# Performance work log

Measured on AMD Instinct MI355X. Metric: run time of the kernel, lower is better.

## Reference

```python
import jax, jax.numpy as jnp
import numpy as np

POP_LUT = jnp.asarray(np.array([bin(i).count('1') for i in range(256)], dtype=np.float32))


def setup_inputs() -> dict:
    key = jax.random.key(0)
    k1, k2, k3, k4 = jax.random.split(key, 4)
    B, k, H, W, d_v = 4, 8, 64, 64, 32
    z = jax.random.uniform(k1, (B, k, H, W), dtype=jnp.float32)
    evidence_mask = jax.random.randint(k2, (B, H * W), 0, 2).astype(bool)
    value_embed = jax.random.normal(k3, (256, d_v), dtype=jnp.float32)
    mask_value = jax.random.normal(k4, (d_v,), dtype=jnp.float32) * 0.1
    temperature = jnp.asarray(1.0, dtype=jnp.float32)
    return {"z": z, "evidence_mask": evidence_mask, "value_embed": value_embed,
            "mask_value": mask_value, "temperature": temperature}


def _bitpack(z):
    # z: (B, k, H, W) -> codes: (B, N) int32 in [0, 2^k)
    B, k, H, W = z.shape
    bits = (z > 0.5).astype(jnp.int32)
    shifts = (2 ** jnp.arange(k, dtype=jnp.int32)).reshape(1, k, 1, 1)
    return (bits * shifts).sum(axis=1).reshape(B, H * W)


def reference(z, evidence_mask, value_embed, mask_value, temperature):
    B, k, H, W = z.shape
    N = H * W
    d_v = value_embed.shape[1]
    codes = _bitpack(z)                                  # (B, N)
    xor = codes[:, :, None] ^ codes[:, None, :]          # (B, N, N)
    dist = POP_LUT[xor]                                  # Hamming distance via LUT
    temp = jnp.maximum(temperature, 0.1)
    scores = -dist / temp
    # gate: keys without evidence are excluded
    scores = jnp.where(evidence_mask[:, None, :], scores, -jnp.inf)
    # if a batch has zero evidence, fall back to uniform attention (scores=0)
    all_masked = ~jnp.any(evidence_mask, axis=-1)        # (B,)
    scores = jnp.where(all_masked[:, None, None], 0.0, scores)
    attn = jax.nn.softmax(scores, axis=-1)               # (B, N, N)
    values = value_embed[jnp.clip(codes, 0, 255)]        # (B, N, d_v)
    values = jnp.where(evidence_mask[:, :, None], values, mask_value[None, None, :])
    ctx = jnp.einsum('bnm,bmd->bnd', attn, values)       # (B, N, d_v)
    return ctx.transpose(0, 2, 1).reshape(B, d_v, H, W)
```

## Files before the change

kernel.cpp:

```cpp
#include <hip/hip_runtime.h>

#define B_   4
#define K_   8
#define N_   4096
#define DV_  32
#define NC_  256

#define WS_OFF_CODES 65536
#define WS_NEEDED    81920

__device__ __forceinline__ int read_mask(const void* m, int layout, int idx) {
    if (layout == 0) return ((const int*)m)[idx] != 0;
    if (layout == 1) return ((const float*)m)[idx] != 0.0f;
    if (layout == 3) return ((const int*)m)[2 * idx] != 0;
    return ((const unsigned char*)m)[idx] != 0;
}

__device__ __forceinline__ int detect_layout(const void* mask, int tid) {
    __shared__ int ok[3];
    if (tid < 3) ok[tid] = 1;
    __syncthreads();
    const unsigned int* mi = (const unsigned int*)mask;
    int li32 = 1, lf32 = 1, li64 = 1;
    for (int i = tid; i < 4096; i += 256) {
        unsigned int v = mi[i];
        li32 &= (v <= 1u);
        lf32 &= (v == 0u || v == 0x3F800000u);
        li64 &= ((i & 1) ? (v == 0u) : (v <= 1u));
    }
    if (!li32) atomicAnd(&ok[0], 0);
    if (!lf32) atomicAnd(&ok[1], 0);
    if (!li64) atomicAnd(&ok[2], 0);
    __syncthreads();
    return ok[2] ? 3 : (ok[0] ? 0 : (ok[1] ? 1 : 2));
}

__global__ void k1_codes_hist(const float* __restrict__ z, const void* mask,
                              int* __restrict__ part, unsigned char* __restrict__ codes) {
    __shared__ int hist[NC_];
    int tid = threadIdx.x;
    int b = blockIdx.x >> 4;
    int n = ((blockIdx.x & 15) << 8) + tid;
    int layout = detect_layout(mask, tid);
    hist[tid] = 0;
    __syncthreads();
    const float* zb = z + (size_t)b * K_ * N_ + n;
    int code = 0;
#pragma unroll
    for (int j = 0; j < K_; ++j) code |= (zb[j * N_] > 0.5f ? 1 : 0) << j;
    codes[b * N_ + n] = (unsigned char)code;
    if (read_mask(mask, layout, b * N_ + n)) atomicAdd(&hist[code], 1);
    __syncthreads();
    part[blockIdx.x * NC_ + tid] = hist[tid];
}

__global__ void __launch_bounds__(256)
k2_ctx_gather(const int* __restrict__ part, const unsigned char* __restrict__ codes,
              const float* __restrict__ V, const float* __restrict__ mv,
              const float* __restrict__ temperature, float* __restrict__ out) {
    __shared__ float X[NC_ * 33];
    __shared__ float CS[NC_];
    __shared__ int red[4];
    int tid = threadIdx.x;
    int b = blockIdx.x >> 4;
    int n0 = (blockIdx.x & 15) << 8;

    int c = 0;
#pragma unroll
    for (int j = 0; j < 16; ++j) c += part[(b * 16 + j) * NC_ + tid];
    CS[tid] = (float)c;

    int s = c;
#pragma unroll
    for (int off = 32; off; off >>= 1) s += __shfl_down(s, off);
    if ((tid & 63) == 0) red[tid >> 6] = s;
    __syncthreads();
    int evid = red[0] + red[1] + red[2] + red[3];

    float temp = fmaxf(temperature[0], 0.1f);
    float t = __expf(-1.0f / temp);

    for (int i = tid; i < NC_ * 33; i += 256) {
        int cc = i / 33, col = i - cc * 33;
        float cf = CS[cc];
        X[i] = (col < DV_) ? cf * V[cc * DV_ + col] : cf;
    }
    __syncthreads();

#pragma unroll
    for (int stg = 0; stg < 8; ++stg) {
        int bit = 1 << stg;
        for (int p = tid; p < 128 * 33; p += 256) {
            int pi = p / 33, col = p - pi * 33;
            int c0 = ((pi >> stg) << (stg + 1)) | (pi & (bit - 1));
            int i0 = c0 * 33 + col, i1 = i0 + bit * 33;
            float x0 = X[i0], x1 = X[i1];
            X[i0] = fmaf(t, x1, x0);
            X[i1] = fmaf(t, x0, x1);
        }
        __syncthreads();
    }

    int code = codes[b * N_ + n0 + tid];
    float* ob = out + (size_t)b * DV_ * N_ + n0 + tid;
    if (evid == 0) {
#pragma unroll
        for (int d = 0; d < DV_; ++d) ob[d * N_] = mv[d];
    } else {
        float rden = 1.0f / X[code * 33 + DV_];
#pragma unroll
        for (int d = 0; d < DV_; ++d) ob[d * N_] = X[code * 33 + d] * rden;
    }
}

__global__ void __launch_bounds__(1024)
fused_all(const float* __restrict__ z, const void* mask, const float* __restrict__ V,
          const float* __restrict__ mask_value, const float* __restrict__ temperature,
          float* __restrict__ out) {
    __shared__ unsigned short codesL[N_];
    __shared__ float csf[NC_];
    __shared__ int cs[NC_];
    __shared__ float ctxL[NC_ * 33];
    __shared__ int ok[3];
    __shared__ int evid_sh;
    int tid = threadIdx.x;
    int b = blockIdx.x;
    if (tid < 3) ok[tid] = 1;
    if (tid == 0) evid_sh = 0;
    if (tid < NC_) cs[tid] = 0;
    __syncthreads();
    {
        const unsigned int* mi = (const unsigned int*)mask;
        int li32 = 1, lf32 = 1, li64 = 1;
        for (int i = tid; i < 4096; i += 1024) {
            unsigned int v = mi[i];
            li32 &= (v <= 1u);
            lf32 &= (v == 0u || v == 0x3F800000u);
            li64 &= ((i & 1) ? (v == 0u) : (v <= 1u));
        }
        if (!li32) atomicAnd(&ok[0], 0);
        if (!lf32) atomicAnd(&ok[1], 0);
        if (!li64) atomicAnd(&ok[2], 0);
    }
    __syncthreads();
    int layout = ok[2] ? 3 : (ok[0] ? 0 : (ok[1] ? 1 : 2));
    for (int i = tid; i < N_; i += 1024) {
        const float* zb = z + (size_t)b * K_ * N_ + i;
        int code = 0;
#pragma unroll
        for (int j = 0; j < K_; ++j) code |= (zb[j * N_] > 0.5f ? 1 : 0) << j;
        codesL[i] = (unsigned short)code;
        if (read_mask(mask, layout, b * N_ + i)) {
            atomicAdd(&cs[code], 1);
            atomicAdd(&evid_sh, 1);
        }
    }
    __syncthreads();
    if (tid < NC_) csf[tid] = (float)cs[tid];
    __syncthreads();
    int evid = evid_sh;
    float temp = fmaxf(temperature[0], 0.1f);
    float rinv = -1.0f / temp;
    int d = tid & 31;
    for (int qi = 0; qi < 8; ++qi) {
        int q = (qi << 5) + (tid >> 5);
        float num = 0.0f, den = 0.0f;
        for (int c = 0; c < NC_; ++c) {
            float cc = csf[c];
            float w = cc * __expf((float)__popc(q ^ c) * rinv);
            den += w;
            num = fmaf(w, V[c * DV_ + d], num);
        }
        ctxL[q * 33 + d] = (evid == 0) ? mask_value[d] : num / den;
    }
    __syncthreads();
    for (int idx = tid; idx < DV_ * N_; idx += 1024) {
        int dd = idx >> 12;
        int n = idx & (N_ - 1);
        out[(size_t)b * DV_ * N_ + idx] = ctxL[codesL[n] * 33 + dd];
    }
}

extern "C" void kernel_launch(void* const* d_in, const int* in_sizes, int n_in,
                              void* d_out, int out_size, void* d_ws, size_t ws_size,
                              hipStream_t stream) {
    const float* z    = (const float*)d_in[0];
    const void*  mask = d_in[1];
    const float* V    = (const float*)d_in[2];
    const float* mv   = (const float*)d_in[3];
    const float* temp = (const float*)d_in[4];
    float* out = (float*)d_out;

    if (ws_size >= (size_t)WS_NEEDED) {
        char* ws = (char*)d_ws;
        int*           part  = (int*)ws;
        unsigned char* codes = (unsigned char*)(ws + WS_OFF_CODES);
        k1_codes_hist<<<B_ * 16, 256, 0, stream>>>(z, mask, part, codes);
        k2_ctx_gather<<<B_ * 16, 256, 0, stream>>>(part, codes, V, mv, temp, out);
    } else {
        fused_all<<<B_, 1024, 0, stream>>>(z, mask, V, mv, temp, out);
    }
}
```

Before: 29.84 us.

## Fuse histogram and context kernels into one launch with redundant per-block histograms

Replaces the two-kernel pipeline (per-slice partial histograms in a workspace, then a gather kernel) with one kernel. Each of the 64 blocks recomputes the full per-batch code histogram from z and the mask, then runs the butterfly transform and writes its slice. This removes one kernel launch and the workspace round trip, but every block now reads all of its batch's z (16x redundant reads) and builds a 4096-element histogram with shared atomics.

```diff
diff --git a/kernel.cpp b/kernel.cpp
--- a/kernel.cpp
+++ b/kernel.cpp
@@ -5,9 +5,6 @@
 #define N_   4096
 #define DV_  32
 #define NC_  256
-
-#define WS_OFF_CODES 65536
-#define WS_NEEDED    81920
 
 __device__ __forceinline__ int read_mask(const void* m, int layout, int idx) {
     if (layout == 0) return ((const int*)m)[idx] != 0;
@@ -35,41 +32,34 @@
     return ok[2] ? 3 : (ok[0] ? 0 : (ok[1] ? 1 : 2));
 }
 
-__global__ void k1_codes_hist(const float* __restrict__ z, const void* mask,
-                              int* __restrict__ part, unsigned char* __restrict__ codes) {
+__global__ void __launch_bounds__(256)
+fused_one(const float* __restrict__ z, const void* mask, const float* __restrict__ V,
+          const float* __restrict__ mv, const float* __restrict__ temperature,
+          float* __restrict__ out) {
+    __shared__ float X[NC_ * 33];
     __shared__ int hist[NC_];
+    __shared__ int red[4];
     int tid = threadIdx.x;
     int b = blockIdx.x >> 4;
-    int n = ((blockIdx.x & 15) << 8) + tid;
+    int slice = blockIdx.x & 15;
+
     int layout = detect_layout(mask, tid);
     hist[tid] = 0;
     __syncthreads();
-    const float* zb = z + (size_t)b * K_ * N_ + n;
-    int code = 0;
+
+    const float* zb = z + (size_t)b * K_ * N_;
+    int mycode = 0;
+    for (int ci = 0; ci < 16; ++ci) {
+        int n = (ci << 8) + tid;
+        int code = 0;
 #pragma unroll
-    for (int j = 0; j < K_; ++j) code |= (zb[j * N_] > 0.5f ? 1 : 0) << j;
-    codes[b * N_ + n] = (unsigned char)code;
-    if (read_mask(mask, layout, b * N_ + n)) atomicAdd(&hist[code], 1);
+        for (int j = 0; j < K_; ++j) code |= (zb[j * N_ + n] > 0.5f ? 1 : 0) << j;
+        if (ci == slice) mycode = code;
+        if (read_mask(mask, layout, b * N_ + n)) atomicAdd(&hist[code], 1);
+    }
     __syncthreads();
-    part[blockIdx.x * NC_ + tid] = hist[tid];
-}
 
-__global__ void __launch_bounds__(256)
-k2_ctx_gather(const int* __restrict__ part, const unsigned char* __restrict__ codes,
-              const float* __restrict__ V, const float* __restrict__ mv,
-              const float* __restrict__ temperature, float* __restrict__ out) {
-    __shared__ float X[NC_ * 33];
-    __shared__ float CS[NC_];
-    __shared__ int red[4];
-    int tid = threadIdx.x;
-    int b = blockIdx.x >> 4;
-    int n0 = (blockIdx.x & 15) << 8;
-
-    int c = 0;
-#pragma unroll
-    for (int j = 0; j < 16; ++j) c += part[(b * 16 + j) * NC_ + tid];
-    CS[tid] = (float)c;
-
+    int c = hist[tid];
     int s = c;
 #pragma unroll
     for (int off = 32; off; off >>= 1) s += __shfl_down(s, off);
@@ -82,7 +72,7 @@
 
     for (int i = tid; i < NC_ * 33; i += 256) {
         int cc = i / 33, col = i - cc * 33;
-        float cf = CS[cc];
+        float cf = (float)hist[cc];
         X[i] = (col < DV_) ? cf * V[cc * DV_ + col] : cf;
     }
     __syncthreads();
@@ -101,83 +91,14 @@
         __syncthreads();
     }
 
-    int code = codes[b * N_ + n0 + tid];
-    float* ob = out + (size_t)b * DV_ * N_ + n0 + tid;
+    float* ob = out + (size_t)b * DV_ * N_ + (slice << 8) + tid;
     if (evid == 0) {
 #pragma unroll
         for (int d = 0; d < DV_; ++d) ob[d * N_] = mv[d];
     } else {
-        float rden = 1.0f / X[code * 33 + DV_];
+        float rden = 1.0f / X[mycode * 33 + DV_];
 #pragma unroll
-        for (int d = 0; d < DV_; ++d) ob[d * N_] = X[code * 33 + d] * rden;
-    }
-}
-
-__global__ void __launch_bounds__(1024)
-fused_all(const float* __restrict__ z, const void* mask, const float* __restrict__ V,
-          const float* __restrict__ mask_value, const float* __restrict__ temperature,
-          float* __restrict__ out) {
-    __shared__ unsigned short codesL[N_];
-    __shared__ float csf[NC_];
-    __shared__ int cs[NC_];
-    __shared__ float ctxL[NC_ * 33];
-    __shared__ int ok[3];
-    __shared__ int evid_sh;
-    int tid = threadIdx.x;
-    int b = blockIdx.x;
-    if (tid < 3) ok[tid] = 1;
-    if (tid == 0) evid_sh = 0;
-    if (tid < NC_) cs[tid] = 0;
-    __syncthreads();
-    {
-        const unsigned int* mi = (const unsigned int*)mask;
-        int li32 = 1, lf32 = 1, li64 = 1;
-        for (int i = tid; i < 4096; i += 1024) {
-            unsigned int v = mi[i];
-            li32 &= (v <= 1u);
-            lf32 &= (v == 0u || v == 0x3F800000u);
-            li64 &= ((i & 1) ? (v == 0u) : (v <= 1u));
-        }
-        if (!li32) atomicAnd(&ok[0], 0);
-        if (!lf32) atomicAnd(&ok[1], 0);
-        if (!li64) atomicAnd(&ok[2], 0);
-    }
-    __syncthreads();
-    int layout = ok[2] ? 3 : (ok[0] ? 0 : (ok[1] ? 1 : 2));
-    for (int i = tid; i < N_; i += 1024) {
-        const float* zb = z + (size_t)b * K_ * N_ + i;
-        int code = 0;
-#pragma unroll
-        for (int j = 0; j < K_; ++j) code |= (zb[j * N_] > 0.5f ? 1 : 0) << j;
-        codesL[i] = (unsigned short)code;
-        if (read_mask(mask, layout, b * N_ + i)) {
-            atomicAdd(&cs[code], 1);
-            atomicAdd(&evid_sh, 1);
-        }
-    }
-    __syncthreads();
-    if (tid < NC_) csf[tid] = (float)cs[tid];
-    __syncthreads();
-    int evid = evid_sh;
-    float temp = fmaxf(temperature[0], 0.1f);
-    float rinv = -1.0f / temp;
-    int d = tid & 31;
-    for (int qi = 0; qi < 8; ++qi) {
-        int q = (qi << 5) + (tid >> 5);
-        float num = 0.0f, den = 0.0f;
-        for (int c = 0; c < NC_; ++c) {
-            float cc = csf[c];
-            float w = cc * __expf((float)__popc(q ^ c) * rinv);
-            den += w;
-            num = fmaf(w, V[c * DV_ + d], num);
-        }
-        ctxL[q * 33 + d] = (evid == 0) ? mask_value[d] : num / den;
-    }
-    __syncthreads();
-    for (int idx = tid; idx < DV_ * N_; idx += 1024) {
-        int dd = idx >> 12;
-        int n = idx & (N_ - 1);
-        out[(size_t)b * DV_ * N_ + idx] = ctxL[codesL[n] * 33 + dd];
+        for (int d = 0; d < DV_; ++d) ob[d * N_] = X[mycode * 33 + d] * rden;
     }
 }
 
@@ -190,14 +111,5 @@
     const float* mv   = (const float*)d_in[3];
     const float* temp = (const float*)d_in[4];
     float* out = (float*)d_out;
-
-    if (ws_size >= (size_t)WS_NEEDED) {
-        char* ws = (char*)d_ws;
-        int*           part  = (int*)ws;
-        unsigned char* codes = (unsigned char*)(ws + WS_OFF_CODES);
-        k1_codes_hist<<<B_ * 16, 256, 0, stream>>>(z, mask, part, codes);
-        k2_ctx_gather<<<B_ * 16, 256, 0, stream>>>(part, codes, V, mv, temp, out);
-    } else {
-        fused_all<<<B_, 1024, 0, stream>>>(z, mask, V, mv, temp, out);
-    }
+    fused_one<<<B_ * 16, 256, 0, stream>>>(z, mask, V, mv, temp, out);
 }
```

Result: slower. 33.35 us (+11.7%).

## Fuse histogram and context kernels into one cooperative launch with grid sync

Applied to the files above, without the earlier changes.

Merges the two-kernel pipeline (per-slice histograms, then Walsh-transform context and gather) into a single cooperative kernel that uses a grid-wide barrier between phases. Each thread keeps its own code in a register, so the codes no longer round-trip through workspace, and one launch gap is removed. It also rewrites the X initialization so each thread fills its own row directly from registers instead of through the shared count array. In exchange it depends on cooperative-launch support and pays for a grid sync; if the launch fails it falls back to the two-kernel path.

```diff
diff --git a/kernel.cpp b/kernel.cpp
--- a/kernel.cpp
+++ b/kernel.cpp
@@ -1,4 +1,7 @@
 #include <hip/hip_runtime.h>
+#include <hip/hip_cooperative_groups.h>
+
+namespace cg = cooperative_groups;
 
 #define B_   4
 #define K_   8
@@ -7,7 +10,8 @@
 #define NC_  256
 
 #define WS_OFF_CODES 65536
-#define WS_NEEDED    81920
+#define WS_COOP      65536
+#define WS_2K        81920
 
 __device__ __forceinline__ int read_mask(const void* m, int layout, int idx) {
     if (layout == 0) return ((const int*)m)[idx] != 0;
@@ -35,40 +39,16 @@
     return ok[2] ? 3 : (ok[0] ? 0 : (ok[1] ? 1 : 2));
 }
 
-__global__ void k1_codes_hist(const float* __restrict__ z, const void* mask,
-                              int* __restrict__ part, unsigned char* __restrict__ codes) {
-    __shared__ int hist[NC_];
-    int tid = threadIdx.x;
-    int b = blockIdx.x >> 4;
-    int n = ((blockIdx.x & 15) << 8) + tid;
-    int layout = detect_layout(mask, tid);
-    hist[tid] = 0;
-    __syncthreads();
-    const float* zb = z + (size_t)b * K_ * N_ + n;
-    int code = 0;
-#pragma unroll
-    for (int j = 0; j < K_; ++j) code |= (zb[j * N_] > 0.5f ? 1 : 0) << j;
-    codes[b * N_ + n] = (unsigned char)code;
-    if (read_mask(mask, layout, b * N_ + n)) atomicAdd(&hist[code], 1);
-    __syncthreads();
-    part[blockIdx.x * NC_ + tid] = hist[tid];
-}
-
-__global__ void __launch_bounds__(256)
-k2_ctx_gather(const int* __restrict__ part, const unsigned char* __restrict__ codes,
-              const float* __restrict__ V, const float* __restrict__ mv,
-              const float* __restrict__ temperature, float* __restrict__ out) {
-    __shared__ float X[NC_ * 33];
-    __shared__ float CS[NC_];
-    __shared__ int red[4];
-    int tid = threadIdx.x;
-    int b = blockIdx.x >> 4;
-    int n0 = (blockIdx.x & 15) << 8;
-
+__device__ __forceinline__ void ctx_and_write(
+        const int* __restrict__ part, int mycode, int b, int slice,
+        const float* __restrict__ V, const float* __restrict__ mv,
+        const float* __restrict__ temperature, float* __restrict__ out,
+        float* X , int* red ) {
+    int tid = threadIdx.x;
     int c = 0;
 #pragma unroll
     for (int j = 0; j < 16; ++j) c += part[(b * 16 + j) * NC_ + tid];
-    CS[tid] = (float)c;
+    float cf = (float)c;
 
     int s = c;
 #pragma unroll
@@ -80,10 +60,10 @@
     float temp = fmaxf(temperature[0], 0.1f);
     float t = __expf(-1.0f / temp);
 
-    for (int i = tid; i < NC_ * 33; i += 256) {
-        int cc = i / 33, col = i - cc * 33;
-        float cf = CS[cc];
-        X[i] = (col < DV_) ? cf * V[cc * DV_ + col] : cf;
+#pragma unroll
+    for (int r = 0; r < 33; ++r) {
+        float v = (r < DV_) ? cf * V[tid * DV_ + r] : cf;
+        X[tid * 33 + r] = v;
     }
     __syncthreads();
 
@@ -101,16 +81,76 @@
         __syncthreads();
     }
 
-    int code = codes[b * N_ + n0 + tid];
-    float* ob = out + (size_t)b * DV_ * N_ + n0 + tid;
+    float* ob = out + (size_t)b * DV_ * N_ + (slice << 8) + tid;
     if (evid == 0) {
 #pragma unroll
         for (int d = 0; d < DV_; ++d) ob[d * N_] = mv[d];
     } else {
-        float rden = 1.0f / X[code * 33 + DV_];
-#pragma unroll
-        for (int d = 0; d < DV_; ++d) ob[d * N_] = X[code * 33 + d] * rden;
-    }
+        float rden = 1.0f / X[mycode * 33 + DV_];
+#pragma unroll
+        for (int d = 0; d < DV_; ++d) ob[d * N_] = X[mycode * 33 + d] * rden;
+    }
+}
+
+__global__ void __launch_bounds__(256)
+coop_one(const float* __restrict__ z, const void* mask, const float* __restrict__ V,
+         const float* __restrict__ mv, const float* __restrict__ temperature,
+         float* __restrict__ out, int* __restrict__ part) {
+    __shared__ float X[NC_ * 33];
+    __shared__ int hist[NC_];
+    __shared__ int red[4];
+    int tid = threadIdx.x;
+    int b = blockIdx.x >> 4;
+    int slice = blockIdx.x & 15;
+    int n = (slice << 8) + tid;
+
+    int layout = detect_layout(mask, tid);
+    hist[tid] = 0;
+    __syncthreads();
+
+    const float* zb = z + (size_t)b * K_ * N_ + n;
+    int mycode = 0;
+#pragma unroll
+    for (int j = 0; j < K_; ++j) mycode |= (zb[j * N_] > 0.5f ? 1 : 0) << j;
+    if (read_mask(mask, layout, b * N_ + n)) atomicAdd(&hist[mycode], 1);
+    __syncthreads();
+    part[blockIdx.x * NC_ + tid] = hist[tid];
+
+    cg::this_grid().sync();
+
+    ctx_and_write(part, mycode, b, slice, V, mv, temperature, out, X, red);
+}
+
+__global__ void k1_codes_hist(const float* __restrict__ z, const void* mask,
+                              int* __restrict__ part, unsigned char* __restrict__ codes) {
+    __shared__ int hist[NC_];
+    int tid = threadIdx.x;
+    int b = blockIdx.x >> 4;
+    int n = ((blockIdx.x & 15) << 8) + tid;
+    int layout = detect_layout(mask, tid);
+    hist[tid] = 0;
+    __syncthreads();
+    const float* zb = z + (size_t)b * K_ * N_ + n;
+    int code = 0;
+#pragma unroll
+    for (int j = 0; j < K_; ++j) code |= (zb[j * N_] > 0.5f ? 1 : 0) << j;
+    codes[b * N_ + n] = (unsigned char)code;
+    if (read_mask(mask, layout, b * N_ + n)) atomicAdd(&hist[code], 1);
+    __syncthreads();
+    part[blockIdx.x * NC_ + tid] = hist[tid];
+}
+
+__global__ void __launch_bounds__(256)
+k2_ctx_gather(const int* __restrict__ part, const unsigned char* __restrict__ codes,
+              const float* __restrict__ V, const float* __restrict__ mv,
+              const float* __restrict__ temperature, float* __restrict__ out) {
+    __shared__ float X[NC_ * 33];
+    __shared__ int red[4];
+    int tid = threadIdx.x;
+    int b = blockIdx.x >> 4;
+    int slice = blockIdx.x & 15;
+    int mycode = codes[b * N_ + (slice << 8) + tid];
+    ctx_and_write(part, mycode, b, slice, V, mv, temperature, out, X, red);
 }
 
 __global__ void __launch_bounds__(1024)
@@ -191,7 +231,17 @@
     const float* temp = (const float*)d_in[4];
     float* out = (float*)d_out;
 
-    if (ws_size >= (size_t)WS_NEEDED) {
+    if (ws_size >= (size_t)WS_COOP) {
+        int* part = (int*)d_ws;
+        void* args[] = {(void*)&z, (void*)&mask, (void*)&V, (void*)&mv,
+                        (void*)&temp, (void*)&out, (void*)&part};
+        hipError_t err = hipLaunchCooperativeKernel((const void*)coop_one,
+                                                    dim3(B_ * 16), dim3(256),
+                                                    args, 0, stream);
+        if (err == hipSuccess) return;
+        (void)hipGetLastError();
+    }
+    if (ws_size >= (size_t)WS_2K) {
         char* ws = (char*)d_ws;
         int*           part  = (int*)ws;
         unsigned char* codes = (unsigned char*)(ws + WS_OFF_CODES);
```

After: 50.88 us. 1.71x slower.
